# Kernel optimization log

Measured on AMD Instinct MI355X. Metric: run time of the kernel, lower is better.

Reference implementation:

```python
import jax, jax.numpy as jnp
import numpy as np

HEADS = 8
CH = 256
DH = CH // HEADS  # 32
NB = 128          # nb_features
EPS = 1e-4


def setup_inputs() -> dict:
    key = jax.random.key(0)
    ks = jax.random.split(key, 8)
    b, c, h, w = 4, CH, 96, 96
    s = 1.0 / np.sqrt(CH)  # typical linear init scale
    x = jax.random.normal(ks[0], (b, c, h, w), dtype=jnp.float32)
    wq = jax.random.normal(ks[1], (CH, CH), dtype=jnp.float32) * s
    wk = jax.random.normal(ks[2], (CH, CH), dtype=jnp.float32) * s
    wv = jax.random.normal(ks[3], (CH, CH), dtype=jnp.float32) * s
    wo = jax.random.normal(ks[4], (CH, CH), dtype=jnp.float32) * s
    bo = jnp.zeros((CH,), dtype=jnp.float32)
    # FAVOR+ gaussian orthogonal random projection (nb_features, dim_head)
    pm = np.random.default_rng(0)
    blocks = []
    for _ in range(NB // DH):
        qmat, _ = np.linalg.qr(pm.standard_normal((DH, DH)))
        blocks.append(qmat.T)
    proj = np.concatenate(blocks, axis=0)
    # scale rows to chi-distributed norms (scaling=0 default in performer_pytorch)
    norms = np.linalg.norm(pm.standard_normal((NB, DH)), axis=1, keepdims=True)
    proj_mat = jnp.asarray(proj * norms, dtype=jnp.float32)
    wp = jax.random.normal(ks[5], (CH, CH, 1, 1), dtype=jnp.float32) * s
    bp = jnp.zeros((CH,), dtype=jnp.float32)
    return {"x": x, "wq": wq, "wk": wk, "wv": wv, "wo": wo, "bo": bo,
            "proj_mat": proj_mat, "wp": wp, "bp": bp}


def softmax_kernel(data, proj, is_query):
    # data: (b, h, n, d); proj: (m, d). Performer FAVOR+ positive softmax features.
    data_normalizer = data.shape[-1] ** -0.25
    ratio = proj.shape[0] ** -0.5
    data_dash = jnp.einsum('bhnd,md->bhnm', data * data_normalizer, proj)
    diag = (jnp.sum(data * data, axis=-1) * 0.5 * (data_normalizer ** 2))[..., None]
    if is_query:
        m = jnp.max(data_dash, axis=-1, keepdims=True)
    else:
        m = jnp.max(data_dash, axis=(-1, -2), keepdims=True)
    return ratio * (jnp.exp(data_dash - diag - m) + EPS)


def reference(x, wq, wk, wv, wo, bo, proj_mat, wp, bp):
    b, c, h, w = x.shape
    n = h * w
    xf = x.reshape(b, c, n).transpose(0, 2, 1)  # (b, n, c)

    def split_heads(t):
        return t.reshape(b, n, HEADS, DH).transpose(0, 2, 1, 3)  # (b, h, n, d)

    q = split_heads(xf @ wq.T)
    k = split_heads(xf @ wk.T)
    v = split_heads(xf @ wv.T)

    qp = softmax_kernel(q, proj_mat, True)   # (b, h, n, m)
    kp = softmax_kernel(k, proj_mat, False)  # (b, h, n, m)

    # non-causal linear attention
    k_sum = jnp.sum(kp, axis=-2)                                   # (b, h, m)
    d_inv = 1.0 / jnp.einsum('bhnm,bhm->bhn', qp, k_sum)           # (b, h, n)
    ctx = jnp.einsum('bhnm,bhnd->bhmd', kp, v)                     # (b, h, m, d)
    out = jnp.einsum('bhnm,bhmd->bhnd', qp, ctx) * d_inv[..., None]

    out = out.transpose(0, 2, 1, 3).reshape(b, n, c)  # merge heads
    out = out @ wo.T + bo                              # to_out (attn_out_bias=True)
    out = out.transpose(0, 2, 1).reshape(b, c, h, w)
    # 1x1 conv projection
    out = jnp.einsum('bchw,oc->bohw', out, wp[:, :, 0, 0]) + bp[None, :, None, None]
    return out
```

## Files before the change

kernel.cpp:

```cpp
#include <hip/hip_runtime.h>

#define NTOT 9216
#define NORMC 0.42044820762685725f
#define RATIO 0.08838834764831845f
#define FEPS 1e-4f

typedef _Float16 h8 __attribute__((ext_vector_type(8)));
typedef float f4 __attribute__((ext_vector_type(4)));

__device__ __forceinline__ void gld16(const _Float16* g, _Float16* l) {
  __builtin_amdgcn_global_load_lds((const __attribute__((address_space(1))) void*)g,
                                   (__attribute__((address_space(3))) void*)l, 16, 0, 0);
}

__global__ __launch_bounds__(256) void prep_small(
    const float* __restrict__ wq, const float* __restrict__ wk,
    const float* __restrict__ wv, const float* __restrict__ proj,
    const float* __restrict__ wo, const float* __restrict__ bo,
    const float* __restrict__ wp, const float* __restrict__ bp,
    _Float16* __restrict__ Wall, _Float16* __restrict__ projh,
    _Float16* __restrict__ Wc, float* __restrict__ bc) {
  int r = blockIdx.x, t = threadIdx.x;
  if (r < 768) {
    const float* src = (r < 256) ? wq + (size_t)r * 256
                     : (r < 512) ? wk + (size_t)(r - 256) * 256
                                 : wv + (size_t)(r - 512) * 256;
    Wall[(size_t)r * 256 + t] = (_Float16)src[t];
  } else if (r < 784) {
    int idx = (r - 768) * 256 + t;
    projh[idx] = (_Float16)proj[idx];
  } else {
    int o = r - 784;
    float acc = 0.f;
    for (int c = 0; c < 256; ++c) acc += wp[o * 256 + c] * wo[c * 256 + t];
    Wc[o * 256 + t] = (_Float16)acc;
    if (t == 0) {
      float ab = bp[o];
      for (int c = 0; c < 256; ++c) ab += wp[o * 256 + c] * bo[c];
      bc[o] = ab;
    }
  }
}

__global__ __launch_bounds__(256) void prep_xT(
    const float* __restrict__ x, _Float16* __restrict__ xT) {
  __shared__ float T_s[64][65];
  int n0 = blockIdx.x * 64, c0 = blockIdx.y * 64, b = blockIdx.z;
  int t = threadIdx.x;
  for (int i = 0; i < 4; ++i) {
    int f = t + i * 256;
    int cc = f >> 4, n4 = f & 15;
    float4 a = *(const float4*)(x + ((size_t)(b * 256 + c0 + cc)) * NTOT + n0 + n4 * 4);
    T_s[cc][n4 * 4 + 0] = a.x;
    T_s[cc][n4 * 4 + 1] = a.y;
    T_s[cc][n4 * 4 + 2] = a.z;
    T_s[cc][n4 * 4 + 3] = a.w;
  }
  __syncthreads();
  for (int i = 0; i < 2; ++i) {
    int f = t + i * 256;
    int nn = f >> 3, c8 = f & 7;
    h8 hv;
    for (int j = 0; j < 8; ++j) hv[j] = (_Float16)T_s[c8 * 8 + j][nn];
    *(h8*)(xT + ((size_t)(b * NTOT + n0 + nn)) * 256 + c0 + c8 * 8) = hv;
  }
}

__global__ __launch_bounds__(256) void qkv_mfma(
    const _Float16* __restrict__ xT, const _Float16* __restrict__ Wall,
    _Float16* __restrict__ q, _Float16* __restrict__ k, _Float16* __restrict__ v) {
  __shared__ __align__(16) _Float16 A_s[128 * 32];
  __shared__ __align__(16) _Float16 B_s[128 * 32];
  int n0 = blockIdx.x * 128;
  int co0 = blockIdx.y * 128;
  int sel = blockIdx.z;
  _Float16* Out = (sel == 0) ? q : (sel == 1) ? k : v;
  const _Float16* Wb = Wall + (size_t)sel * 65536;
  int t = threadIdx.x, wave = t >> 6, lane = t & 63;
  int lm = lane & 15, lg = lane >> 4;
  int wm = (wave & 1) * 64, wn = (wave >> 1) * 64;
  const _Float16* gA = xT + (size_t)(n0 + wave * 32 + (lane >> 2)) * 256 + (lane & 3) * 8;
  const _Float16* gB = Wb + (size_t)(co0 + wave * 32 + (lane >> 2)) * 256 + (lane & 3) * 8;
  _Float16* lA = A_s + wave * 1024;
  _Float16* lB = B_s + wave * 1024;
  f4 acc[4][4] = {};
  for (int kt = 0; kt < 8; ++kt) {
    int c0 = kt * 32;
    __syncthreads();
    gld16(gA + c0, lA);
    gld16(gA + c0 + 16 * 256, lA + 512);
    gld16(gB + c0, lB);
    gld16(gB + c0 + 16 * 256, lB + 512);
    __syncthreads();
    h8 a[4], bf[4];
#pragma unroll
    for (int mi = 0; mi < 4; ++mi) a[mi] = *(const h8*)&A_s[(wm + mi * 16 + lm) * 32 + lg * 8];
#pragma unroll
    for (int ni = 0; ni < 4; ++ni) bf[ni] = *(const h8*)&B_s[(wn + ni * 16 + lm) * 32 + lg * 8];
#pragma unroll
    for (int mi = 0; mi < 4; ++mi)
#pragma unroll
      for (int ni = 0; ni < 4; ++ni)
        acc[mi][ni] = __builtin_amdgcn_mfma_f32_16x16x32_f16(a[mi], bf[ni], acc[mi][ni], 0, 0, 0);
  }
#pragma unroll
  for (int mi = 0; mi < 4; ++mi)
#pragma unroll
    for (int ni = 0; ni < 4; ++ni)
#pragma unroll
      for (int r = 0; r < 4; ++r)
        Out[(size_t)(n0 + wm + mi * 16 + lg * 4 + r) * 256 + co0 + wn + ni * 16 + lm] =
            (_Float16)acc[mi][ni][r];
}

__global__ __launch_bounds__(256) void kmax_mfma(
    const _Float16* __restrict__ k, const _Float16* __restrict__ projh,
    float* __restrict__ kmaxp, float* __restrict__ ctx_aug) {
  __shared__ __align__(16) _Float16 k_s[128 * 32];
  __shared__ float red4[4];
  int bh = blockIdx.y, b = bh >> 3, h = bh & 7;
  int nbase = blockIdx.x * 512;
  int t = threadIdx.x, wave = t >> 6, lane = t & 63, lm = lane & 15, lg = lane >> 4;
  if (blockIdx.x == 0) {
#pragma unroll
    for (int i = 0; i < 18; ++i) ctx_aug[(size_t)bh * 4608 + t + i * 256] = 0.f;
  }
  h8 pr[8];
#pragma unroll
  for (int mt = 0; mt < 8; ++mt) pr[mt] = *(const h8*)&projh[(mt * 16 + lm) * 32 + lg * 8];
  const _Float16* gK =
      k + ((size_t)(b * NTOT + nbase + wave * 32 + (lane >> 2))) * 256 + h * 32 + (lane & 3) * 8;
  _Float16* lK = k_s + wave * 1024;
  float vmax = -1e30f;
  for (int ch = 0; ch < 4; ++ch) {
    __syncthreads();
    gld16(gK + (size_t)ch * 128 * 256, lK);
    gld16(gK + (size_t)ch * 128 * 256 + 16 * 256, lK + 512);
    __syncthreads();
#pragma unroll
    for (int nt = 0; nt < 2; ++nt) {
      h8 a = *(const h8*)&k_s[(wave * 32 + nt * 16 + lm) * 32 + lg * 8];
#pragma unroll
      for (int mt = 0; mt < 8; ++mt) {
        f4 z = {0.f, 0.f, 0.f, 0.f};
        f4 d = __builtin_amdgcn_mfma_f32_16x16x32_f16(a, pr[mt], z, 0, 0, 0);
        vmax = fmaxf(vmax, fmaxf(fmaxf(d[0], d[1]), fmaxf(d[2], d[3])));
      }
    }
  }
  for (int i = 1; i < 64; i <<= 1) vmax = fmaxf(vmax, __shfl_xor(vmax, i, 64));
  if (lane == 0) red4[wave] = vmax;
  __syncthreads();
  if (t == 0)
    kmaxp[bh * 18 + blockIdx.x] =
        NORMC * fmaxf(fmaxf(red4[0], red4[1]), fmaxf(red4[2], red4[3]));
}

__global__ __launch_bounds__(256) void ctx_mfma(
    const _Float16* __restrict__ k, const _Float16* __restrict__ v,
    const _Float16* __restrict__ projh, const float* __restrict__ kmaxp,
    float* __restrict__ ctx_aug) {
  __shared__ __align__(16) _Float16 k_s[128 * 32];
  __shared__ __align__(16) _Float16 vT_s[32 * 136];
  __shared__ __align__(16) _Float16 kpT[128 * 136];
  __shared__ float tmp_s[256];
  __shared__ float kmax_sh;
  int bh = blockIdx.y, b = bh >> 3, h = bh & 7;
  int nbase = blockIdx.x * 512;
  int t = threadIdx.x, wave = t >> 6, lane = t & 63, lm = lane & 15, lg = lane >> 4;
  h8 pr[8];
#pragma unroll
  for (int mt = 0; mt < 8; ++mt) pr[mt] = *(const h8*)&projh[(mt * 16 + lm) * 32 + lg * 8];
  if (t == 0) {
    float mx = -1e30f;
    for (int i = 0; i < 18; ++i) mx = fmaxf(mx, kmaxp[bh * 18 + i]);
    kmax_sh = mx;
  }
  __syncthreads();
  float kmax = kmax_sh;
  const _Float16* gK =
      k + ((size_t)(b * NTOT + nbase + wave * 32 + (lane >> 2))) * 256 + h * 32 + (lane & 3) * 8;
  _Float16* lK = k_s + wave * 1024;
  f4 cacc[2][2] = {};
  float ksacc = 0.f;
  for (int ch = 0; ch < 4; ++ch) {
    int n0 = nbase + ch * 128;
    gld16(gK + (size_t)ch * 128 * 256, lK);
    gld16(gK + (size_t)ch * 128 * 256 + 16 * 256, lK + 512);
#pragma unroll
    for (int i = 0; i < 2; ++i) {
      int f = t + i * 256;
      int row = f >> 2, c = f & 3;
      h8 vv = *(const h8*)(v + ((size_t)(b * NTOT + n0 + row)) * 256 + h * 32 + c * 8);
#pragma unroll
      for (int j = 0; j < 8; ++j) vT_s[(c * 8 + j) * 136 + row] = vv[j];
    }
    __syncthreads();
    if (t < 128) {
      float s = 0.f;
#pragma unroll
      for (int c = 0; c < 4; ++c) {
        h8 kv = *(const h8*)&k_s[t * 32 + c * 8];
#pragma unroll
        for (int j = 0; j < 8; ++j) s += (float)kv[j] * (float)kv[j];
      }
      tmp_s[t] = s * (0.5f * NORMC * NORMC);
    }
    f4 dsh[2][8];
#pragma unroll
    for (int nt = 0; nt < 2; ++nt) {
      h8 a = *(const h8*)&k_s[(wave * 32 + nt * 16 + lm) * 32 + lg * 8];
#pragma unroll
      for (int mt = 0; mt < 8; ++mt) {
        f4 z = {0.f, 0.f, 0.f, 0.f};
        dsh[nt][mt] = __builtin_amdgcn_mfma_f32_16x16x32_f16(a, pr[mt], z, 0, 0, 0);
      }
    }
    __syncthreads();
#pragma unroll
    for (int nt = 0; nt < 2; ++nt)
#pragma unroll
      for (int mt = 0; mt < 8; ++mt)
#pragma unroll
        for (int r = 0; r < 4; ++r) {
          int nl = wave * 32 + nt * 16 + lg * 4 + r;
          float val = RATIO * (__expf(NORMC * dsh[nt][mt][r] - tmp_s[nl] - kmax) + FEPS);
          kpT[(mt * 16 + lm) * 136 + nl] = (_Float16)val;
        }
    __syncthreads();
#pragma unroll
    for (int k2 = 0; k2 < 4; ++k2) {
      h8 a2[2], b2[2];
#pragma unroll
      for (int mt2 = 0; mt2 < 2; ++mt2)
        a2[mt2] = *(const h8*)&kpT[(wave * 32 + mt2 * 16 + lm) * 136 + k2 * 32 + lg * 8];
#pragma unroll
      for (int dt = 0; dt < 2; ++dt)
        b2[dt] = *(const h8*)&vT_s[(dt * 16 + lm) * 136 + k2 * 32 + lg * 8];
#pragma unroll
      for (int mt2 = 0; mt2 < 2; ++mt2)
#pragma unroll
        for (int dt = 0; dt < 2; ++dt)
          cacc[mt2][dt] =
              __builtin_amdgcn_mfma_f32_16x16x32_f16(a2[mt2], b2[dt], cacc[mt2][dt], 0, 0, 0);
    }
    {
      int m = t & 127, half = t >> 7;
#pragma unroll
      for (int j = 0; j < 8; ++j) {
        h8 kv = *(const h8*)&kpT[m * 136 + half * 64 + j * 8];
#pragma unroll
        for (int e = 0; e < 8; ++e) ksacc += (float)kv[e];
      }
    }
    __syncthreads();
  }
  float* cb = ctx_aug + (size_t)bh * 4608;
#pragma unroll
  for (int mt2 = 0; mt2 < 2; ++mt2)
#pragma unroll
    for (int dt = 0; dt < 2; ++dt)
#pragma unroll
      for (int r = 0; r < 4; ++r)
        atomicAdd(&cb[(wave * 32 + mt2 * 16 + lg * 4 + r) * 36 + dt * 16 + lm],
                  cacc[mt2][dt][r]);
  tmp_s[t] = ksacc;
  __syncthreads();
  if (t < 128) atomicAdd(&cb[t * 36 + 32], tmp_s[t] + tmp_s[t + 128]);
}

__global__ __launch_bounds__(256) void attn_mfma(
    const _Float16* __restrict__ q, const _Float16* __restrict__ projh,
    const float* __restrict__ ctx_aug, _Float16* __restrict__ attn) {
  __shared__ __align__(16) _Float16 q_sh[128 * 32];
  __shared__ __align__(16) _Float16 qp_s[128 * 136];
  __shared__ __align__(16) _Float16 ctxT[32 * 136];
  __shared__ float diag_s[128], den_s[128], ksum_s[128];
  int n0 = blockIdx.x * 128;
  int bh = blockIdx.y, b = bh >> 3, h = bh & 7;
  int t = threadIdx.x, wave = t >> 6, lane = t & 63, lm = lane & 15, lg = lane >> 4;
  const float* cb = ctx_aug + (size_t)bh * 4608;
  h8 pr[8];
#pragma unroll
  for (int mt = 0; mt < 8; ++mt) pr[mt] = *(const h8*)&projh[(mt * 16 + lm) * 32 + lg * 8];
  const _Float16* gQ =
      q + ((size_t)(b * NTOT + n0 + wave * 32 + (lane >> 2))) * 256 + h * 32 + (lane & 3) * 8;
  gld16(gQ, q_sh + wave * 1024);
  gld16(gQ + 16 * 256, q_sh + wave * 1024 + 512);
  {
    int m = t >> 1, dbase = (t & 1) * 16;
#pragma unroll
    for (int g = 0; g < 4; ++g) {
      float4 cv = *(const float4*)(cb + m * 36 + dbase + g * 4);
      ctxT[(dbase + g * 4 + 0) * 136 + m] = (_Float16)cv.x;
      ctxT[(dbase + g * 4 + 1) * 136 + m] = (_Float16)cv.y;
      ctxT[(dbase + g * 4 + 2) * 136 + m] = (_Float16)cv.z;
      ctxT[(dbase + g * 4 + 3) * 136 + m] = (_Float16)cv.w;
    }
  }
  if (t < 128) ksum_s[t] = cb[t * 36 + 32];
  __syncthreads();
  if (t < 128) {
    float s = 0.f;
#pragma unroll
    for (int c = 0; c < 4; ++c) {
      h8 qv = *(const h8*)&q_sh[t * 32 + c * 8];
#pragma unroll
      for (int j = 0; j < 8; ++j) s += (float)qv[j] * (float)qv[j];
    }
    diag_s[t] = s * (0.5f * NORMC * NORMC);
  }
  f4 dsh[2][8];
#pragma unroll
  for (int nt = 0; nt < 2; ++nt) {
    h8 a = *(const h8*)&q_sh[(wave * 32 + nt * 16 + lm) * 32 + lg * 8];
#pragma unroll
    for (int mt = 0; mt < 8; ++mt) {
      f4 z = {0.f, 0.f, 0.f, 0.f};
      dsh[nt][mt] = __builtin_amdgcn_mfma_f32_16x16x32_f16(a, pr[mt], z, 0, 0, 0);
    }
  }
  __syncthreads();
#pragma unroll
  for (int nt = 0; nt < 2; ++nt) {
    float mx[4];
#pragma unroll
    for (int r = 0; r < 4; ++r) {
      float m0 = -1e30f;
#pragma unroll
      for (int mt = 0; mt < 8; ++mt) m0 = fmaxf(m0, dsh[nt][mt][r]);
      for (int i = 1; i < 16; i <<= 1) m0 = fmaxf(m0, __shfl_xor(m0, i, 64));
      mx[r] = m0;
    }
#pragma unroll
    for (int mt = 0; mt < 8; ++mt)
#pragma unroll
      for (int r = 0; r < 4; ++r) {
        int nl = wave * 32 + nt * 16 + lg * 4 + r;
        float val =
            RATIO * (__expf(NORMC * dsh[nt][mt][r] - diag_s[nl] - NORMC * mx[r]) + FEPS);
        qp_s[nl * 136 + mt * 16 + lm] = (_Float16)val;
      }
  }
  __syncthreads();
  if (t < 128) {
    float s = 0.f;
#pragma unroll
    for (int j = 0; j < 16; ++j) {
      h8 qv = *(const h8*)&qp_s[t * 136 + j * 8];
#pragma unroll
      for (int e = 0; e < 8; ++e) s += (float)qv[e] * ksum_s[j * 8 + e];
    }
    den_s[t] = 1.f / s;
  }
  f4 oacc[2][2] = {};
#pragma unroll
  for (int k2 = 0; k2 < 4; ++k2) {
    h8 a2[2], b2[2];
#pragma unroll
    for (int nt = 0; nt < 2; ++nt)
      a2[nt] = *(const h8*)&qp_s[(wave * 32 + nt * 16 + lm) * 136 + k2 * 32 + lg * 8];
#pragma unroll
    for (int dt = 0; dt < 2; ++dt)
      b2[dt] = *(const h8*)&ctxT[(dt * 16 + lm) * 136 + k2 * 32 + lg * 8];
#pragma unroll
    for (int nt = 0; nt < 2; ++nt)
#pragma unroll
      for (int dt = 0; dt < 2; ++dt)
        oacc[nt][dt] = __builtin_amdgcn_mfma_f32_16x16x32_f16(a2[nt], b2[dt], oacc[nt][dt], 0, 0, 0);
  }
  __syncthreads();
#pragma unroll
  for (int nt = 0; nt < 2; ++nt)
#pragma unroll
    for (int dt = 0; dt < 2; ++dt)
#pragma unroll
      for (int r = 0; r < 4; ++r) {
        int nl = wave * 32 + nt * 16 + lg * 4 + r;
        float di = den_s[nl];
        attn[((size_t)(b * NTOT + n0 + nl)) * 256 + h * 32 + dt * 16 + lm] =
            (_Float16)(oacc[nt][dt][r] * di);
      }
}

__global__ __launch_bounds__(256) void out_mfma(
    const _Float16* __restrict__ Wc, const _Float16* __restrict__ attn,
    const float* __restrict__ bc, float* __restrict__ out) {
  __shared__ __align__(16) _Float16 A_s[128 * 32];
  __shared__ __align__(16) _Float16 B_s[128 * 32];
  int bx = blockIdx.x;
  int o0 = blockIdx.y * 128;
  int b = bx / 72, nb0 = (bx % 72) * 128;
  int t = threadIdx.x, wave = t >> 6, lane = t & 63;
  int lm = lane & 15, lg = lane >> 4;
  int wm = (wave & 1) * 64, wn = (wave >> 1) * 64;
  const _Float16* gA = Wc + (size_t)(o0 + wave * 32 + (lane >> 2)) * 256 + (lane & 3) * 8;
  const _Float16* gB =
      attn + (size_t)(b * NTOT + nb0 + wave * 32 + (lane >> 2)) * 256 + (lane & 3) * 8;
  _Float16* lA = A_s + wave * 1024;
  _Float16* lB = B_s + wave * 1024;
  f4 acc[4][4] = {};
  for (int kt = 0; kt < 8; ++kt) {
    int c0 = kt * 32;
    __syncthreads();
    gld16(gA + c0, lA);
    gld16(gA + c0 + 16 * 256, lA + 512);
    gld16(gB + c0, lB);
    gld16(gB + c0 + 16 * 256, lB + 512);
    __syncthreads();
    h8 a[4], bf[4];
#pragma unroll
    for (int mi = 0; mi < 4; ++mi) a[mi] = *(const h8*)&A_s[(wm + mi * 16 + lm) * 32 + lg * 8];
#pragma unroll
    for (int ni = 0; ni < 4; ++ni) bf[ni] = *(const h8*)&B_s[(wn + ni * 16 + lm) * 32 + lg * 8];
#pragma unroll
    for (int mi = 0; mi < 4; ++mi)
#pragma unroll
      for (int ni = 0; ni < 4; ++ni)
        acc[mi][ni] = __builtin_amdgcn_mfma_f32_16x16x32_f16(a[mi], bf[ni], acc[mi][ni], 0, 0, 0);
  }
  float bias[4][4];
#pragma unroll
  for (int mi = 0; mi < 4; ++mi)
#pragma unroll
    for (int r = 0; r < 4; ++r) bias[mi][r] = bc[o0 + wm + mi * 16 + lg * 4 + r];
#pragma unroll
  for (int mi = 0; mi < 4; ++mi)
#pragma unroll
    for (int ni = 0; ni < 4; ++ni)
#pragma unroll
      for (int r = 0; r < 4; ++r) {
        int o = o0 + wm + mi * 16 + lg * 4 + r;
        int n = nb0 + wn + ni * 16 + lm;
        out[((size_t)(b * 256 + o)) * NTOT + n] = acc[mi][ni][r] + bias[mi][r];
      }
}

extern "C" void kernel_launch(void* const* d_in, const int* in_sizes, int n_in,
                              void* d_out, int out_size, void* d_ws, size_t ws_size,
                              hipStream_t stream) {
  const float* x = (const float*)d_in[0];
  const float* wq = (const float*)d_in[1];
  const float* wk = (const float*)d_in[2];
  const float* wv = (const float*)d_in[3];
  const float* wo = (const float*)d_in[4];
  const float* bo = (const float*)d_in[5];
  const float* proj = (const float*)d_in[6];
  const float* wp = (const float*)d_in[7];
  const float* bp = (const float*)d_in[8];
  float* out = (float*)d_out;
  float* ws = (float*)d_ws;

  float* ctx_aug = ws;
  float* kmaxp = ctx_aug + 147456;
  float* bc = kmaxp + 576;
  _Float16* hb = (_Float16*)(bc + 256);
  const size_t THALF = (size_t)4 * NTOT * 256;
  _Float16* q_h = hb;
  _Float16* k_h = q_h + THALF;
  _Float16* v_h = k_h + THALF;
  _Float16* xT = v_h + THALF;
  _Float16* Wall = xT + THALF;
  _Float16* Wc = Wall + 768 * 256;
  _Float16* projh = Wc + 65536;

  prep_small<<<1040, 256, 0, stream>>>(wq, wk, wv, proj, wo, bo, wp, bp, Wall, projh, Wc, bc);
  prep_xT<<<dim3(144, 4, 4), 256, 0, stream>>>(x, xT);
  qkv_mfma<<<dim3(288, 2, 3), 256, 0, stream>>>(xT, Wall, q_h, k_h, v_h);
  kmax_mfma<<<dim3(18, 32), 256, 0, stream>>>(k_h, projh, kmaxp, ctx_aug);
  ctx_mfma<<<dim3(18, 32), 256, 0, stream>>>(k_h, v_h, projh, kmaxp, ctx_aug);
  attn_mfma<<<dim3(72, 32), 256, 0, stream>>>(q_h, projh, ctx_aug, xT);
  out_mfma<<<dim3(288, 2), 256, 0, stream>>>(Wc, xT, bc, out);
}
```

Baseline: 222.6 us.

## Swizzle LDS tiles, vectorize stores, replace ctx atomics with partial reduction, pre-transpose V

Applies an XOR swizzle to the LDS tiles in every MFMA kernel so that fragment reads avoid bank conflicts. The qkv and output GEMMs swap their MFMA operands so each lane can store packed h4/float4 results instead of scalars. V is now transposed once into a global buffer by a new kernel, and ctx_mfma writes per-block partial sums that a new reduce kernel combines, replacing float atomics; k-sum is also accumulated in registers. attn_mfma keeps the diag, max and denominator in registers with fewer barriers, and kmax and ctx use more, smaller blocks. The cost is two extra launches, an extra transpose pass over V, and a larger workspace.

Measured after the change: 252.2 us. 13.3% more time.

```diff
diff --git a/kernel.cpp b/kernel.cpp
--- a/kernel.cpp
+++ b/kernel.cpp
@@ -6,6 +6,7 @@
 #define FEPS 1e-4f
 
 typedef _Float16 h8 __attribute__((ext_vector_type(8)));
+typedef _Float16 h4 __attribute__((ext_vector_type(4)));
 typedef float f4 __attribute__((ext_vector_type(4)));
 
 __device__ __forceinline__ void gld16(const _Float16* g, _Float16* l) {
@@ -71,18 +72,19 @@
     _Float16* __restrict__ q, _Float16* __restrict__ k, _Float16* __restrict__ v) {
   __shared__ __align__(16) _Float16 A_s[128 * 32];
   __shared__ __align__(16) _Float16 B_s[128 * 32];
-  int n0 = blockIdx.x * 128;
-  int co0 = blockIdx.y * 128;
-  int sel = blockIdx.z;
+  int n0 = blockIdx.x * 128, co0 = blockIdx.y * 128, sel = blockIdx.z;
   _Float16* Out = (sel == 0) ? q : (sel == 1) ? k : v;
   const _Float16* Wb = Wall + (size_t)sel * 65536;
   int t = threadIdx.x, wave = t >> 6, lane = t & 63;
   int lm = lane & 15, lg = lane >> 4;
   int wm = (wave & 1) * 64, wn = (wave >> 1) * 64;
-  const _Float16* gA = xT + (size_t)(n0 + wave * 32 + (lane >> 2)) * 256 + (lane & 3) * 8;
-  const _Float16* gB = Wb + (size_t)(co0 + wave * 32 + (lane >> 2)) * 256 + (lane & 3) * 8;
+  int srow = wave * 32 + (lane >> 2);
+  int scol = ((lane & 3) ^ ((lane >> 3) & 3)) * 8;
+  const _Float16* gA = Wb + (size_t)(co0 + srow) * 256 + scol;
+  const _Float16* gB = xT + (size_t)(n0 + srow) * 256 + scol;
   _Float16* lA = A_s + wave * 1024;
   _Float16* lB = B_s + wave * 1024;
+  int pg = (lg ^ ((lm >> 1) & 3)) * 8;
   f4 acc[4][4] = {};
   for (int kt = 0; kt < 8; ++kt) {
     int c0 = kt * 32;
@@ -94,9 +96,9 @@
     __syncthreads();
     h8 a[4], bf[4];
 #pragma unroll
-    for (int mi = 0; mi < 4; ++mi) a[mi] = *(const h8*)&A_s[(wm + mi * 16 + lm) * 32 + lg * 8];
-#pragma unroll
-    for (int ni = 0; ni < 4; ++ni) bf[ni] = *(const h8*)&B_s[(wn + ni * 16 + lm) * 32 + lg * 8];
+    for (int mi = 0; mi < 4; ++mi) a[mi] = *(const h8*)&A_s[(wm + mi * 16 + lm) * 32 + pg];
+#pragma unroll
+    for (int ni = 0; ni < 4; ++ni) bf[ni] = *(const h8*)&B_s[(wn + ni * 16 + lm) * 32 + pg];
 #pragma unroll
     for (int mi = 0; mi < 4; ++mi)
 #pragma unroll
@@ -106,40 +108,59 @@
 #pragma unroll
   for (int mi = 0; mi < 4; ++mi)
 #pragma unroll
-    for (int ni = 0; ni < 4; ++ni)
-#pragma unroll
-      for (int r = 0; r < 4; ++r)
-        Out[(size_t)(n0 + wm + mi * 16 + lg * 4 + r) * 256 + co0 + wn + ni * 16 + lm] =
-            (_Float16)acc[mi][ni][r];
+    for (int ni = 0; ni < 4; ++ni) {
+      h4 hv;
+#pragma unroll
+      for (int r = 0; r < 4; ++r) hv[r] = (_Float16)acc[mi][ni][r];
+      *(h4*)(Out + (size_t)(n0 + wn + ni * 16 + lm) * 256 + co0 + wm + mi * 16 + lg * 4) = hv;
+    }
+}
+
+__global__ __launch_bounds__(256) void prep_vT(
+    const _Float16* __restrict__ v, _Float16* __restrict__ vT) {
+  __shared__ _Float16 T[64 * 132];
+  int n0 = blockIdx.x * 128, c0 = blockIdx.y * 64, b = blockIdx.z;
+  int t = threadIdx.x;
+  for (int i = 0; i < 4; ++i) {
+    int f = t + i * 256;
+    int nl = f >> 3, cg = f & 7;
+    h8 vv = *(const h8*)(v + ((size_t)(b * NTOT + n0 + nl)) * 256 + c0 + cg * 8);
+#pragma unroll
+    for (int j = 0; j < 8; ++j) T[(cg * 8 + j) * 132 + nl] = vv[j];
+  }
+  __syncthreads();
+  int cl = t >> 2, seg = t & 3;
+  _Float16* gout = vT + ((size_t)(b * 256 + c0 + cl)) * NTOT + n0 + seg * 32;
+#pragma unroll
+  for (int j = 0; j < 8; ++j)
+    *(h4*)(gout + j * 4) = *(const h4*)&T[cl * 132 + seg * 32 + j * 4];
 }
 
 __global__ __launch_bounds__(256) void kmax_mfma(
     const _Float16* __restrict__ k, const _Float16* __restrict__ projh,
-    float* __restrict__ kmaxp, float* __restrict__ ctx_aug) {
+    float* __restrict__ kmaxp) {
   __shared__ __align__(16) _Float16 k_s[128 * 32];
   __shared__ float red4[4];
   int bh = blockIdx.y, b = bh >> 3, h = bh & 7;
-  int nbase = blockIdx.x * 512;
+  int nbase = blockIdx.x * 256;
   int t = threadIdx.x, wave = t >> 6, lane = t & 63, lm = lane & 15, lg = lane >> 4;
-  if (blockIdx.x == 0) {
-#pragma unroll
-    for (int i = 0; i < 18; ++i) ctx_aug[(size_t)bh * 4608 + t + i * 256] = 0.f;
-  }
   h8 pr[8];
 #pragma unroll
   for (int mt = 0; mt < 8; ++mt) pr[mt] = *(const h8*)&projh[(mt * 16 + lm) * 32 + lg * 8];
+  int scol = ((lane & 3) ^ ((lane >> 3) & 3)) * 8;
   const _Float16* gK =
-      k + ((size_t)(b * NTOT + nbase + wave * 32 + (lane >> 2))) * 256 + h * 32 + (lane & 3) * 8;
+      k + ((size_t)(b * NTOT + nbase + wave * 32 + (lane >> 2))) * 256 + h * 32 + scol;
   _Float16* lK = k_s + wave * 1024;
+  int pg = (lg ^ ((lm >> 1) & 3)) * 8;
   float vmax = -1e30f;
-  for (int ch = 0; ch < 4; ++ch) {
-    __syncthreads();
-    gld16(gK + (size_t)ch * 128 * 256, lK);
-    gld16(gK + (size_t)ch * 128 * 256 + 16 * 256, lK + 512);
+  for (int ch = 0; ch < 2; ++ch) {
+    __syncthreads();
+    gld16(gK + (size_t)(ch * 128) * 256, lK);
+    gld16(gK + (size_t)(ch * 128) * 256 + 16 * 256, lK + 512);
     __syncthreads();
 #pragma unroll
     for (int nt = 0; nt < 2; ++nt) {
-      h8 a = *(const h8*)&k_s[(wave * 32 + nt * 16 + lm) * 32 + lg * 8];
+      h8 a = *(const h8*)&k_s[(wave * 32 + nt * 16 + lm) * 32 + pg];
 #pragma unroll
       for (int mt = 0; mt < 8; ++mt) {
         f4 z = {0.f, 0.f, 0.f, 0.f};
@@ -152,48 +173,50 @@
   if (lane == 0) red4[wave] = vmax;
   __syncthreads();
   if (t == 0)
-    kmaxp[bh * 18 + blockIdx.x] =
+    kmaxp[bh * 36 + blockIdx.x] =
         NORMC * fmaxf(fmaxf(red4[0], red4[1]), fmaxf(red4[2], red4[3]));
 }
 
 __global__ __launch_bounds__(256) void ctx_mfma(
-    const _Float16* __restrict__ k, const _Float16* __restrict__ v,
+    const _Float16* __restrict__ k, const _Float16* __restrict__ vT,
     const _Float16* __restrict__ projh, const float* __restrict__ kmaxp,
-    float* __restrict__ ctx_aug) {
+    float* __restrict__ part) {
   __shared__ __align__(16) _Float16 k_s[128 * 32];
   __shared__ __align__(16) _Float16 vT_s[32 * 136];
   __shared__ __align__(16) _Float16 kpT[128 * 136];
-  __shared__ float tmp_s[256];
+  __shared__ float diag_s[128];
   __shared__ float kmax_sh;
   int bh = blockIdx.y, b = bh >> 3, h = bh & 7;
-  int nbase = blockIdx.x * 512;
+  int nbase = blockIdx.x * 384;
   int t = threadIdx.x, wave = t >> 6, lane = t & 63, lm = lane & 15, lg = lane >> 4;
   h8 pr[8];
 #pragma unroll
   for (int mt = 0; mt < 8; ++mt) pr[mt] = *(const h8*)&projh[(mt * 16 + lm) * 32 + lg * 8];
   if (t == 0) {
     float mx = -1e30f;
-    for (int i = 0; i < 18; ++i) mx = fmaxf(mx, kmaxp[bh * 18 + i]);
+    for (int i = 0; i < 36; ++i) mx = fmaxf(mx, kmaxp[bh * 36 + i]);
     kmax_sh = mx;
   }
   __syncthreads();
   float kmax = kmax_sh;
+  int scol = ((lane & 3) ^ ((lane >> 3) & 3)) * 8;
   const _Float16* gK =
-      k + ((size_t)(b * NTOT + nbase + wave * 32 + (lane >> 2))) * 256 + h * 32 + (lane & 3) * 8;
+      k + ((size_t)(b * NTOT + nbase + wave * 32 + (lane >> 2))) * 256 + h * 32 + scol;
+  const _Float16* gV = vT + ((size_t)(b * 256 + h * 32 + (t >> 3))) * NTOT + nbase;
   _Float16* lK = k_s + wave * 1024;
+  int pg = (lg ^ ((lm >> 1) & 3)) * 8;
   f4 cacc[2][2] = {};
-  float ksacc = 0.f;
-  for (int ch = 0; ch < 4; ++ch) {
-    int n0 = nbase + ch * 128;
-    gld16(gK + (size_t)ch * 128 * 256, lK);
-    gld16(gK + (size_t)ch * 128 * 256 + 16 * 256, lK + 512);
-#pragma unroll
-    for (int i = 0; i < 2; ++i) {
-      int f = t + i * 256;
-      int row = f >> 2, c = f & 3;
-      h8 vv = *(const h8*)(v + ((size_t)(b * NTOT + n0 + row)) * 256 + h * 32 + c * 8);
-#pragma unroll
-      for (int j = 0; j < 8; ++j) vT_s[(c * 8 + j) * 136 + row] = vv[j];
+  float ks[8] = {};
+  for (int ch = 0; ch < 3; ++ch) {
+    gld16(gK + (size_t)(ch * 128) * 256, lK);
+    gld16(gK + (size_t)(ch * 128) * 256 + 16 * 256, lK + 512);
+    {
+      int d = t >> 3, g = t & 7;
+#pragma unroll
+      for (int i = 0; i < 2; ++i) {
+        h8 vv = *(const h8*)(gV + ch * 128 + (i * 8 + g) * 8);
+        *(h8*)&vT_s[d * 136 + (i * 8 + g) * 8] = vv;
+      }
     }
     __syncthreads();
     if (t < 128) {
@@ -204,12 +227,12 @@
 #pragma unroll
         for (int j = 0; j < 8; ++j) s += (float)kv[j] * (float)kv[j];
       }
-      tmp_s[t] = s * (0.5f * NORMC * NORMC);
+      diag_s[t] = s * (0.5f * NORMC * NORMC);
     }
     f4 dsh[2][8];
 #pragma unroll
     for (int nt = 0; nt < 2; ++nt) {
-      h8 a = *(const h8*)&k_s[(wave * 32 + nt * 16 + lm) * 32 + lg * 8];
+      h8 a = *(const h8*)&k_s[(wave * 32 + nt * 16 + lm) * 32 + pg];
 #pragma unroll
       for (int mt = 0; mt < 8; ++mt) {
         f4 z = {0.f, 0.f, 0.f, 0.f};
@@ -220,13 +243,19 @@
 #pragma unroll
     for (int nt = 0; nt < 2; ++nt)
 #pragma unroll
-      for (int mt = 0; mt < 8; ++mt)
+      for (int mt = 0; mt < 8; ++mt) {
+        h4 hv;
+        float lsum = 0.f;
 #pragma unroll
         for (int r = 0; r < 4; ++r) {
           int nl = wave * 32 + nt * 16 + lg * 4 + r;
-          float val = RATIO * (__expf(NORMC * dsh[nt][mt][r] - tmp_s[nl] - kmax) + FEPS);
-          kpT[(mt * 16 + lm) * 136 + nl] = (_Float16)val;
+          float val = RATIO * (__expf(NORMC * dsh[nt][mt][r] - diag_s[nl] - kmax) + FEPS);
+          hv[r] = (_Float16)val;
+          lsum += val;
         }
+        ks[mt] += lsum;
+        *(h4*)&kpT[(mt * 16 + lm) * 136 + wave * 32 + nt * 16 + lg * 4] = hv;
+      }
     __syncthreads();
 #pragma unroll
     for (int k2 = 0; k2 < 4; ++k2) {
@@ -244,29 +273,40 @@
           cacc[mt2][dt] =
               __builtin_amdgcn_mfma_f32_16x16x32_f16(a2[mt2], b2[dt], cacc[mt2][dt], 0, 0, 0);
     }
-    {
-      int m = t & 127, half = t >> 7;
-#pragma unroll
-      for (int j = 0; j < 8; ++j) {
-        h8 kv = *(const h8*)&kpT[m * 136 + half * 64 + j * 8];
-#pragma unroll
-        for (int e = 0; e < 8; ++e) ksacc += (float)kv[e];
-      }
-    }
-    __syncthreads();
-  }
-  float* cb = ctx_aug + (size_t)bh * 4608;
+    __syncthreads();
+  }
+  float* pp = part + (size_t)(blockIdx.y * 24 + blockIdx.x) * 4224;
 #pragma unroll
   for (int mt2 = 0; mt2 < 2; ++mt2)
 #pragma unroll
     for (int dt = 0; dt < 2; ++dt)
-#pragma unroll
-      for (int r = 0; r < 4; ++r)
-        atomicAdd(&cb[(wave * 32 + mt2 * 16 + lg * 4 + r) * 36 + dt * 16 + lm],
-                  cacc[mt2][dt][r]);
-  tmp_s[t] = ksacc;
-  __syncthreads();
-  if (t < 128) atomicAdd(&cb[t * 36 + 32], tmp_s[t] + tmp_s[t + 128]);
+      *(f4*)(pp + (dt * 16 + lm) * 128 + wave * 32 + mt2 * 16 + lg * 4) = cacc[mt2][dt];
+  float* redk = (float*)kpT;
+#pragma unroll
+  for (int mt = 0; mt < 8; ++mt) {
+    float s = ks[mt];
+    s += __shfl_xor(s, 16, 64);
+    s += __shfl_xor(s, 32, 64);
+    if (lg == 0) redk[wave * 128 + mt * 16 + lm] = s;
+  }
+  __syncthreads();
+  if (t < 128)
+    pp[32 * 128 + t] = redk[t] + redk[128 + t] + redk[256 + t] + redk[384 + t];
+}
+
+__global__ __launch_bounds__(256) void reduce_ctx(
+    const float* __restrict__ part, float* __restrict__ ctx_aug) {
+  int bh = blockIdx.x, t = threadIdx.x;
+  const float* pb = part + (size_t)bh * 24 * 4224;
+  for (int it = 0; it < 17; ++it) {
+    int cell = t + it * 256;
+    if (cell < 4224) {
+      float s = 0.f;
+      for (int p = 0; p < 24; ++p) s += pb[(size_t)p * 4224 + cell];
+      int d = cell >> 7, m = cell & 127;
+      ctx_aug[(size_t)bh * 4608 + m * 36 + d] = s;
+    }
+  }
 }
 
 __global__ __launch_bounds__(256) void attn_mfma(
@@ -275,7 +315,7 @@
   __shared__ __align__(16) _Float16 q_sh[128 * 32];
   __shared__ __align__(16) _Float16 qp_s[128 * 136];
   __shared__ __align__(16) _Float16 ctxT[32 * 136];
-  __shared__ float diag_s[128], den_s[128], ksum_s[128];
+  __shared__ float ksum_s[128];
   int n0 = blockIdx.x * 128;
   int bh = blockIdx.y, b = bh >> 3, h = bh & 7;
   int t = threadIdx.x, wave = t >> 6, lane = t & 63, lm = lane & 15, lg = lane >> 4;
@@ -283,8 +323,9 @@
   h8 pr[8];
 #pragma unroll
   for (int mt = 0; mt < 8; ++mt) pr[mt] = *(const h8*)&projh[(mt * 16 + lm) * 32 + lg * 8];
+  int scol = ((lane & 3) ^ ((lane >> 3) & 3)) * 8;
   const _Float16* gQ =
-      q + ((size_t)(b * NTOT + n0 + wave * 32 + (lane >> 2))) * 256 + h * 32 + (lane & 3) * 8;
+      q + ((size_t)(b * NTOT + n0 + wave * 32 + (lane >> 2))) * 256 + h * 32 + scol;
   gld16(gQ, q_sh + wave * 1024);
   gld16(gQ + 16 * 256, q_sh + wave * 1024 + 512);
   {
@@ -300,87 +341,83 @@
   }
   if (t < 128) ksum_s[t] = cb[t * 36 + 32];
   __syncthreads();
-  if (t < 128) {
+  int pg = (lg ^ ((lm >> 1) & 3)) * 8;
+  float diag_r[2];
+#pragma unroll
+  for (int nt = 0; nt < 2; ++nt) {
+    int n = wave * 32 + nt * 16 + lm;
     float s = 0.f;
 #pragma unroll
     for (int c = 0; c < 4; ++c) {
-      h8 qv = *(const h8*)&q_sh[t * 32 + c * 8];
+      h8 qv = *(const h8*)&q_sh[n * 32 + c * 8];
 #pragma unroll
       for (int j = 0; j < 8; ++j) s += (float)qv[j] * (float)qv[j];
     }
-    diag_s[t] = s * (0.5f * NORMC * NORMC);
+    diag_r[nt] = s * (0.5f * NORMC * NORMC);
   }
   f4 dsh[2][8];
 #pragma unroll
   for (int nt = 0; nt < 2; ++nt) {
-    h8 a = *(const h8*)&q_sh[(wave * 32 + nt * 16 + lm) * 32 + lg * 8];
+    h8 qf = *(const h8*)&q_sh[(wave * 32 + nt * 16 + lm) * 32 + pg];
 #pragma unroll
     for (int mt = 0; mt < 8; ++mt) {
       f4 z = {0.f, 0.f, 0.f, 0.f};
-      dsh[nt][mt] = __builtin_amdgcn_mfma_f32_16x16x32_f16(a, pr[mt], z, 0, 0, 0);
-    }
-  }
-  __syncthreads();
+      dsh[nt][mt] = __builtin_amdgcn_mfma_f32_16x16x32_f16(pr[mt], qf, z, 0, 0, 0);
+    }
+  }
+  float den_r[2];
 #pragma unroll
   for (int nt = 0; nt < 2; ++nt) {
-    float mx[4];
-#pragma unroll
-    for (int r = 0; r < 4; ++r) {
-      float m0 = -1e30f;
-#pragma unroll
-      for (int mt = 0; mt < 8; ++mt) m0 = fmaxf(m0, dsh[nt][mt][r]);
-      for (int i = 1; i < 16; i <<= 1) m0 = fmaxf(m0, __shfl_xor(m0, i, 64));
-      mx[r] = m0;
-    }
+    float mx = -1e30f;
 #pragma unroll
     for (int mt = 0; mt < 8; ++mt)
 #pragma unroll
+      for (int r = 0; r < 4; ++r) mx = fmaxf(mx, dsh[nt][mt][r]);
+    mx = fmaxf(mx, __shfl_xor(mx, 16, 64));
+    mx = fmaxf(mx, __shfl_xor(mx, 32, 64));
+    float den = 0.f;
+#pragma unroll
+    for (int mt = 0; mt < 8; ++mt) {
+      h4 hv;
+#pragma unroll
       for (int r = 0; r < 4; ++r) {
-        int nl = wave * 32 + nt * 16 + lg * 4 + r;
-        float val =
-            RATIO * (__expf(NORMC * dsh[nt][mt][r] - diag_s[nl] - NORMC * mx[r]) + FEPS);
-        qp_s[nl * 136 + mt * 16 + lm] = (_Float16)val;
+        float val = RATIO * (__expf(NORMC * (dsh[nt][mt][r] - mx) - diag_r[nt]) + FEPS);
+        hv[r] = (_Float16)val;
+        den += val * ksum_s[mt * 16 + lg * 4 + r];
       }
-  }
-  __syncthreads();
-  if (t < 128) {
-    float s = 0.f;
-#pragma unroll
-    for (int j = 0; j < 16; ++j) {
-      h8 qv = *(const h8*)&qp_s[t * 136 + j * 8];
-#pragma unroll
-      for (int e = 0; e < 8; ++e) s += (float)qv[e] * ksum_s[j * 8 + e];
-    }
-    den_s[t] = 1.f / s;
-  }
+      *(h4*)&qp_s[(wave * 32 + nt * 16 + lm) * 136 + mt * 16 + lg * 4] = hv;
+    }
+    den += __shfl_xor(den, 16, 64);
+    den += __shfl_xor(den, 32, 64);
+    den_r[nt] = 1.f / den;
+  }
+  __syncthreads();
   f4 oacc[2][2] = {};
 #pragma unroll
   for (int k2 = 0; k2 < 4; ++k2) {
-    h8 a2[2], b2[2];
+    h8 ac[2], bq[2];
+#pragma unroll
+    for (int dt = 0; dt < 2; ++dt)
+      ac[dt] = *(const h8*)&ctxT[(dt * 16 + lm) * 136 + k2 * 32 + lg * 8];
 #pragma unroll
     for (int nt = 0; nt < 2; ++nt)
-      a2[nt] = *(const h8*)&qp_s[(wave * 32 + nt * 16 + lm) * 136 + k2 * 32 + lg * 8];
+      bq[nt] = *(const h8*)&qp_s[(wave * 32 + nt * 16 + lm) * 136 + k2 * 32 + lg * 8];
 #pragma unroll
     for (int dt = 0; dt < 2; ++dt)
-      b2[dt] = *(const h8*)&ctxT[(dt * 16 + lm) * 136 + k2 * 32 + lg * 8];
-#pragma unroll
-    for (int nt = 0; nt < 2; ++nt)
-#pragma unroll
-      for (int dt = 0; dt < 2; ++dt)
-        oacc[nt][dt] = __builtin_amdgcn_mfma_f32_16x16x32_f16(a2[nt], b2[dt], oacc[nt][dt], 0, 0, 0);
-  }
-  __syncthreads();
-#pragma unroll
-  for (int nt = 0; nt < 2; ++nt)
-#pragma unroll
-    for (int dt = 0; dt < 2; ++dt)
-#pragma unroll
-      for (int r = 0; r < 4; ++r) {
-        int nl = wave * 32 + nt * 16 + lg * 4 + r;
-        float di = den_s[nl];
-        attn[((size_t)(b * NTOT + n0 + nl)) * 256 + h * 32 + dt * 16 + lm] =
-            (_Float16)(oacc[nt][dt][r] * di);
-      }
+#pragma unroll
+      for (int nt = 0; nt < 2; ++nt)
+        oacc[dt][nt] = __builtin_amdgcn_mfma_f32_16x16x32_f16(ac[dt], bq[nt], oacc[dt][nt], 0, 0, 0);
+  }
+#pragma unroll
+  for (int dt = 0; dt < 2; ++dt)
+#pragma unroll
+    for (int nt = 0; nt < 2; ++nt) {
+      int n = wave * 32 + nt * 16 + lm;
+      h4 hv;
+#pragma unroll
+      for (int r = 0; r < 4; ++r) hv[r] = (_Float16)(oacc[dt][nt][r] * den_r[nt]);
+      *(h4*)(attn + ((size_t)(b * NTOT + n0 + n)) * 256 + h * 32 + dt * 16 + lg * 4) = hv;
+    }
 }
 
 __global__ __launch_bounds__(256) void out_mfma(
@@ -394,11 +431,13 @@
   int t = threadIdx.x, wave = t >> 6, lane = t & 63;
   int lm = lane & 15, lg = lane >> 4;
   int wm = (wave & 1) * 64, wn = (wave >> 1) * 64;
-  const _Float16* gA = Wc + (size_t)(o0 + wave * 32 + (lane >> 2)) * 256 + (lane & 3) * 8;
-  const _Float16* gB =
-      attn + (size_t)(b * NTOT + nb0 + wave * 32 + (lane >> 2)) * 256 + (lane & 3) * 8;
+  int srow = wave * 32 + (lane >> 2);
+  int scol = ((lane & 3) ^ ((lane >> 3) & 3)) * 8;
+  const _Float16* gA = Wc + (size_t)(o0 + srow) * 256 + scol;
+  const _Float16* gB = attn + (size_t)(b * NTOT + nb0 + srow) * 256 + scol;
   _Float16* lA = A_s + wave * 1024;
   _Float16* lB = B_s + wave * 1024;
+  int pg = (lg ^ ((lm >> 1) & 3)) * 8;
   f4 acc[4][4] = {};
   for (int kt = 0; kt < 8; ++kt) {
     int c0 = kt * 32;
@@ -410,30 +449,26 @@
     __syncthreads();
     h8 a[4], bf[4];
 #pragma unroll
-    for (int mi = 0; mi < 4; ++mi) a[mi] = *(const h8*)&A_s[(wm + mi * 16 + lm) * 32 + lg * 8];
-#pragma unroll
-    for (int ni = 0; ni < 4; ++ni) bf[ni] = *(const h8*)&B_s[(wn + ni * 16 + lm) * 32 + lg * 8];
+    for (int mi = 0; mi < 4; ++mi) a[mi] = *(const h8*)&A_s[(wm + mi * 16 + lm) * 32 + pg];
+#pragma unroll
+    for (int ni = 0; ni < 4; ++ni) bf[ni] = *(const h8*)&B_s[(wn + ni * 16 + lm) * 32 + pg];
 #pragma unroll
     for (int mi = 0; mi < 4; ++mi)
 #pragma unroll
       for (int ni = 0; ni < 4; ++ni)
-        acc[mi][ni] = __builtin_amdgcn_mfma_f32_16x16x32_f16(a[mi], bf[ni], acc[mi][ni], 0, 0, 0);
-  }
-  float bias[4][4];
-#pragma unroll
-  for (int mi = 0; mi < 4; ++mi)
-#pragma unroll
-    for (int r = 0; r < 4; ++r) bias[mi][r] = bc[o0 + wm + mi * 16 + lg * 4 + r];
-#pragma unroll
-  for (int mi = 0; mi < 4; ++mi)
-#pragma unroll
-    for (int ni = 0; ni < 4; ++ni)
-#pragma unroll
-      for (int r = 0; r < 4; ++r) {
-        int o = o0 + wm + mi * 16 + lg * 4 + r;
-        int n = nb0 + wn + ni * 16 + lm;
-        out[((size_t)(b * 256 + o)) * NTOT + n] = acc[mi][ni][r] + bias[mi][r];
-      }
+        acc[mi][ni] = __builtin_amdgcn_mfma_f32_16x16x32_f16(bf[ni], a[mi], acc[mi][ni], 0, 0, 0);
+  }
+#pragma unroll
+  for (int mi = 0; mi < 4; ++mi) {
+    int o = o0 + wm + mi * 16 + lm;
+    float bias = bc[o];
+#pragma unroll
+    for (int ni = 0; ni < 4; ++ni) {
+      f4 ov = acc[mi][ni];
+      float4 st = make_float4(ov[0] + bias, ov[1] + bias, ov[2] + bias, ov[3] + bias);
+      *(float4*)(out + ((size_t)(b * 256 + o)) * NTOT + nb0 + wn + ni * 16 + lg * 4) = st;
+    }
+  }
 }
 
 extern "C" void kernel_launch(void* const* d_in, const int* in_sizes, int n_in,
@@ -451,24 +486,28 @@
   float* out = (float*)d_out;
   float* ws = (float*)d_ws;
 
-  float* ctx_aug = ws;
+  float* part = ws;
+  float* ctx_aug = part + 3244032;
   float* kmaxp = ctx_aug + 147456;
-  float* bc = kmaxp + 576;
+  float* bc = kmaxp + 1152;
   _Float16* hb = (_Float16*)(bc + 256);
   const size_t THALF = (size_t)4 * NTOT * 256;
   _Float16* q_h = hb;
   _Float16* k_h = q_h + THALF;
   _Float16* v_h = k_h + THALF;
   _Float16* xT = v_h + THALF;
-  _Float16* Wall = xT + THALF;
+  _Float16* vTg = xT + THALF;
+  _Float16* Wall = vTg + THALF;
   _Float16* Wc = Wall + 768 * 256;
   _Float16* projh = Wc + 65536;
 
   prep_small<<<1040, 256, 0, stream>>>(wq, wk, wv, proj, wo, bo, wp, bp, Wall, projh, Wc, bc);
   prep_xT<<<dim3(144, 4, 4), 256, 0, stream>>>(x, xT);
   qkv_mfma<<<dim3(288, 2, 3), 256, 0, stream>>>(xT, Wall, q_h, k_h, v_h);
-  kmax_mfma<<<dim3(18, 32), 256, 0, stream>>>(k_h, projh, kmaxp, ctx_aug);
-  ctx_mfma<<<dim3(18, 32), 256, 0, stream>>>(k_h, v_h, projh, kmaxp, ctx_aug);
+  prep_vT<<<dim3(72, 4, 4), 256, 0, stream>>>(v_h, vTg);
+  kmax_mfma<<<dim3(36, 32), 256, 0, stream>>>(k_h, projh, kmaxp);
+  ctx_mfma<<<dim3(24, 32), 256, 0, stream>>>(k_h, vTg, projh, kmaxp, part);
+  reduce_ctx<<<32, 256, 0, stream>>>(part, ctx_aug);
   attn_mfma<<<dim3(72, 32), 256, 0, stream>>>(q_h, projh, ctx_aug, xT);
   out_mfma<<<dim3(288, 2), 256, 0, stream>>>(Wc, xT, bc, out);
 }
```
